# Kernel optimization log

Measured on AMD Instinct MI355X. Metric: run time of the kernel, lower is better.

Reference implementation:

```python
import jax, jax.numpy as jnp
import numpy as np

P = 4        # number of sequence pairs (half batch)
L = 512      # sequence length
D = 64       # embedding dim
NUM_CLASSES = 4
BIAS_INIT = 10.0


def setup_inputs() -> dict:
    key = jax.random.key(0)
    k1, k2, k3 = jax.random.split(key, 3)
    seqs_logits = jax.random.normal(k1, (2 * P, L, D), dtype=jnp.float32)
    ordinal_weight = jax.random.normal(k2, (1, NUM_CLASSES), dtype=jnp.float32)
    ordinal_bias = jax.random.normal(k3, (NUM_CLASSES,), dtype=jnp.float32) + BIAS_INIT
    return {"seqs_logits": seqs_logits, "ordinal_weight": ordinal_weight,
            "ordinal_bias": ordinal_bias}


def reference(seqs_logits, ordinal_weight, ordinal_bias):
    half = seqs_logits.shape[0] // 2
    z0 = seqs_logits[:half]          # [P, L0, D]
    z1 = seqs_logits[half:2 * half]  # [P, L1, D]

    def score_plus(z0_i, z1_i):
        # pairwise negative L1 distance: [L0, L1]
        s = -jnp.sum(jnp.abs(z0_i[:, None, :] - z1_i[None, :, :]), axis=-1)
        a = jax.nn.softmax(s, axis=1)   # row-wise alignment
        b = jax.nn.softmax(s, axis=0)   # column-wise alignment
        c = a + b - a * b               # symmetric soft alignment
        c_val = jnp.sum(c * s) / jnp.sum(c)
        logit = c_val * ordinal_weight + ordinal_bias  # [1, 4]
        return logit.reshape(-1)        # [4]

    return jax.vmap(score_plus)(z0, z1)  # [P, 4]
```

## Files before the change

kernel.cpp:

```cpp
#include <hip/hip_runtime.h>
#include <math.h>

#define P 4
#define L 512
#define D 64
#define NC 4
#define RS 68
#define SHIFT 64.0f

#define COLP_O  0
#define RA1_O   16384
#define RA2_O   32768
#define RAB1_O  49152
#define RAB2_O  65536
#define BP_O    81920

__device__ __forceinline__ void stage2(const float* __restrict__ z, int pair, int jb, int kb,
                                       int tid, float (*jt)[RS], float (*kt)[RS]) {
    const float4* z0t = (const float4*)(z + ((size_t)pair * L + jb * 64) * D);
    const float4* z1t = (const float4*)(z + ((size_t)(P + pair) * L + kb * 64) * D);
    #pragma unroll
    for (int i = 0; i < 4; ++i) {
        const int li = i * 256 + tid;
        const float4 a = z0t[li];
        const float4 b = z1t[li];
        *(float4*)&jt[li >> 4][(li & 15) * 4] = a;
        *(float4*)&kt[li >> 4][(li & 15) * 4] = b;
    }
}

__device__ __forceinline__ void dist16(const float (*bt)[RS], const float (*vt)[RS],
                                       int ty, int tx, float acc[4][4]) {
    #pragma unroll
    for (int r = 0; r < 4; ++r)
        #pragma unroll
        for (int q = 0; q < 4; ++q) acc[r][q] = 0.f;
    #pragma unroll
    for (int c = 0; c < 16; ++c) {
        float4 bv[4], vv[4];
        #pragma unroll
        for (int r = 0; r < 4; ++r) bv[r] = *(const float4*)&bt[ty + 16 * r][c * 4];
        #pragma unroll
        for (int q = 0; q < 4; ++q) vv[q] = *(const float4*)&vt[tx + 16 * q][c * 4];
        #pragma unroll
        for (int r = 0; r < 4; ++r)
            #pragma unroll
            for (int q = 0; q < 4; ++q)
                acc[r][q] += fabsf(bv[r].x - vv[q].x) + fabsf(bv[r].y - vv[q].y)
                           + fabsf(bv[r].z - vv[q].z) + fabsf(bv[r].w - vv[q].w);
    }
}

__global__ __launch_bounds__(256) void col_pass(const float* __restrict__ z, float* __restrict__ ws) {
    const int bx = blockIdx.x;
    const int pair = bx >> 6, kb = (bx >> 3) & 7, jb = bx & 7;
    const int tid = threadIdx.x, tx = tid & 15, ty = tid >> 4;
    __shared__ float jt[64][RS], kt[64][RS];
    stage2(z, pair, jb, kb, tid, jt, kt);
    __syncthreads();

    float acc[4][4];
    dist16(kt, jt, ty, tx, acc);

    float csum[4];
    #pragma unroll
    for (int r = 0; r < 4; ++r) {
        float s = 0.f;
        #pragma unroll
        for (int q = 0; q < 4; ++q) s += __expf(SHIFT - acc[r][q]);
        csum[r] = s;
    }
    #pragma unroll
    for (int off = 1; off <= 8; off <<= 1)
        #pragma unroll
        for (int r = 0; r < 4; ++r) csum[r] += __shfl_xor(csum[r], off);
    if (tx == 0) {
        #pragma unroll
        for (int r = 0; r < 4; ++r)
            ws[COLP_O + (pair * 8 + jb) * 512 + kb * 64 + ty + 16 * r] = csum[r];
    }
}

__global__ __launch_bounds__(256) void row_pass(const float* __restrict__ z, float* __restrict__ ws) {
    const int bx = blockIdx.x;
    const int pair = bx >> 6, kb = (bx >> 3) & 7, jb = bx & 7;
    const int tid = threadIdx.x, tx = tid & 15, ty = tid >> 4;
    __shared__ float jt[64][RS], kt[64][RS];
    __shared__ float ctmp[64][4];
    __shared__ float crcp_s[64];
    __shared__ float bred[4][2];

    stage2(z, pair, jb, kb, tid, jt, kt);
    {
        const int kl = tid >> 2, q = tid & 3;
        ctmp[kl][q] = ws[COLP_O + (pair * 8 + 2 * q) * 512 + kb * 64 + kl]
                    + ws[COLP_O + (pair * 8 + 2 * q + 1) * 512 + kb * 64 + kl];
    }
    __syncthreads();
    if (tid < 64)
        crcp_s[tid] = 1.0f / (ctmp[tid][0] + ctmp[tid][1] + ctmp[tid][2] + ctmp[tid][3]);
    __syncthreads();

    float crcp[4];
    #pragma unroll
    for (int q = 0; q < 4; ++q) crcp[q] = crcp_s[tx + 16 * q];

    float acc[4][4];
    dist16(jt, kt, ty, tx, acc);

    float A1[4], A2[4], AB1[4], AB2[4], Bs = 0.f, Bc = 0.f;
    #pragma unroll
    for (int r = 0; r < 4; ++r) { A1[r] = A2[r] = AB1[r] = AB2[r] = 0.f; }
    #pragma unroll
    for (int r = 0; r < 4; ++r) {
        #pragma unroll
        for (int q = 0; q < 4; ++q) {
            const float sv = -acc[r][q];
            const float e  = __expf(SHIFT + sv);
            const float b  = e * crcp[q];
            const float eb = e * b;
            A1[r]  += e * sv;   A2[r]  += e;
            AB1[r] += eb * sv;  AB2[r] += eb;
            Bs += b * sv;       Bc += b;
        }
    }
    #pragma unroll
    for (int off = 1; off <= 8; off <<= 1) {
        #pragma unroll
        for (int r = 0; r < 4; ++r) {
            A1[r]  += __shfl_xor(A1[r],  off);
            A2[r]  += __shfl_xor(A2[r],  off);
            AB1[r] += __shfl_xor(AB1[r], off);
            AB2[r] += __shfl_xor(AB2[r], off);
        }
    }
    if (tx == 0) {
        #pragma unroll
        for (int r = 0; r < 4; ++r) {
            const int idx = (pair * 8 + kb) * 512 + jb * 64 + ty + 16 * r;
            ws[RA1_O + idx]  = A1[r];
            ws[RA2_O + idx]  = A2[r];
            ws[RAB1_O + idx] = AB1[r];
            ws[RAB2_O + idx] = AB2[r];
        }
    }
    #pragma unroll
    for (int off = 1; off <= 32; off <<= 1) {
        Bs += __shfl_xor(Bs, off);
        Bc += __shfl_xor(Bc, off);
    }
    const int wave = tid >> 6, lane = tid & 63;
    if (lane == 0) { bred[wave][0] = Bs; bred[wave][1] = Bc; }
    __syncthreads();
    if (tid == 0) {
        const int bidp = kb * 8 + jb;
        ws[BP_O + (pair * 64 + bidp) * 2]     = bred[0][0] + bred[1][0] + bred[2][0] + bred[3][0];
        ws[BP_O + (pair * 64 + bidp) * 2 + 1] = bred[0][1] + bred[1][1] + bred[2][1] + bred[3][1];
    }
}

__global__ __launch_bounds__(256) void finalize(const float* __restrict__ ws,
                                                const float* __restrict__ w,
                                                const float* __restrict__ bias,
                                                float* __restrict__ out) {
    const int pair = blockIdx.x;
    const int tid = threadIdx.x;
    float cs = 0.f, cc = 0.f;
    #pragma unroll
    for (int jj = 0; jj < 2; ++jj) {
        const int j = tid + jj * 256;
        float A1 = 0.f, A2 = 0.f, AB1 = 0.f, AB2 = 0.f;
        #pragma unroll
        for (int kb = 0; kb < 8; ++kb) {
            const int idx = (pair * 8 + kb) * 512 + j;
            A1  += ws[RA1_O + idx];
            A2  += ws[RA2_O + idx];
            AB1 += ws[RAB1_O + idx];
            AB2 += ws[RAB2_O + idx];
        }
        const float r = 1.0f / A2;
        cs += (A1 - AB1) * r;
        cc += 1.0f - AB2 * r;
    }
    if (tid < 64) {
        cs += ws[BP_O + (pair * 64 + tid) * 2];
        cc += ws[BP_O + (pair * 64 + tid) * 2 + 1];
    }
    #pragma unroll
    for (int off = 1; off <= 32; off <<= 1) {
        cs += __shfl_xor(cs, off);
        cc += __shfl_xor(cc, off);
    }
    __shared__ float red[4][2];
    const int wave = tid >> 6, lane = tid & 63;
    if (lane == 0) { red[wave][0] = cs; red[wave][1] = cc; }
    __syncthreads();
    if (tid == 0) {
        const float tcs = red[0][0] + red[1][0] + red[2][0] + red[3][0];
        const float tcc = red[0][1] + red[1][1] + red[2][1] + red[3][1];
        const float c_val = tcs / tcc;
        #pragma unroll
        for (int cls = 0; cls < NC; ++cls)
            out[pair * NC + cls] = c_val * w[cls] + bias[cls];
    }
}

extern "C" void kernel_launch(void* const* d_in, const int* in_sizes, int n_in,
                              void* d_out, int out_size, void* d_ws, size_t ws_size,
                              hipStream_t stream) {
    const float* z    = (const float*)d_in[0];
    const float* w    = (const float*)d_in[1];
    const float* bias = (const float*)d_in[2];
    float* out = (float*)d_out;
    float* ws  = (float*)d_ws;

    col_pass<<<dim3(P * 64), dim3(256), 0, stream>>>(z, ws);
    row_pass<<<dim3(P * 64), dim3(256), 0, stream>>>(z, ws);
    finalize<<<dim3(P),      dim3(256), 0, stream>>>(ws, w, bias, out);
}
```

Measured before the change: 75.39 us.

## Compute distance matrix once, store it, and accumulate alignment in second pass

Instead of computing the L1 distance tile twice (once for column sums, once for row stats), a single kernel computes distances, writes them to workspace, and emits both row and column exp partial sums. A second kernel reloads the stored distances, forms the full symmetric alignment c directly with row and column reciprocals, and reduces c*s and c per block. Finalize becomes one block handling all pairs. This trades a second distance computation for an 8 MB write and read of the score matrix through global memory.

```diff
diff --git a/kernel.cpp b/kernel.cpp
--- a/kernel.cpp
+++ b/kernel.cpp
@@ -8,149 +8,147 @@
 #define RS 68
 #define SHIFT 64.0f
 
-#define COLP_O  0
-#define RA1_O   16384
-#define RA2_O   32768
-#define RAB1_O  49152
-#define RAB2_O  65536
-#define BP_O    81920
+#define COLP_O 0
+#define ROWP_O 16384
+#define BP_O   32768
+#define SV_O   33280
 
-__device__ __forceinline__ void stage2(const float* __restrict__ z, int pair, int jb, int kb,
-                                       int tid, float (*jt)[RS], float (*kt)[RS]) {
-    const float4* z0t = (const float4*)(z + ((size_t)pair * L + jb * 64) * D);
-    const float4* z1t = (const float4*)(z + ((size_t)(P + pair) * L + kb * 64) * D);
-    #pragma unroll
-    for (int i = 0; i < 4; ++i) {
-        const int li = i * 256 + tid;
-        const float4 a = z0t[li];
-        const float4 b = z1t[li];
-        *(float4*)&jt[li >> 4][(li & 15) * 4] = a;
-        *(float4*)&kt[li >> 4][(li & 15) * 4] = b;
+__global__ __launch_bounds__(256) void dist_stats(const float* __restrict__ z,
+                                                  float* __restrict__ ws) {
+    const int bx = blockIdx.x;
+    const int pair = bx >> 6, kb = (bx >> 3) & 7, jb = bx & 7;
+    const int tid = threadIdx.x, tx = tid & 15, ty = tid >> 4;
+    const int wave = tid >> 6, lane = tid & 63;
+
+    __shared__ float jt[64][RS], kt[64][RS];
+    __shared__ float csred[4][64];
+
+    {
+        const float4* z0t = (const float4*)(z + ((size_t)pair * L + jb * 64) * D);
+        const float4* z1t = (const float4*)(z + ((size_t)(P + pair) * L + kb * 64) * D);
+        #pragma unroll
+        for (int i = 0; i < 4; ++i) {
+            const int li = i * 256 + tid;
+            const float4 a = z0t[li];
+            const float4 b = z1t[li];
+            *(float4*)&jt[li >> 4][(li & 15) * 4] = a;
+            *(float4*)&kt[li >> 4][(li & 15) * 4] = b;
+        }
     }
-}
+    __syncthreads();
 
-__device__ __forceinline__ void dist16(const float (*bt)[RS], const float (*vt)[RS],
-                                       int ty, int tx, float acc[4][4]) {
+    float acc[4][4];
     #pragma unroll
     for (int r = 0; r < 4; ++r)
         #pragma unroll
         for (int q = 0; q < 4; ++q) acc[r][q] = 0.f;
     #pragma unroll
     for (int c = 0; c < 16; ++c) {
-        float4 bv[4], vv[4];
+        float4 jv[4], kv[4];
         #pragma unroll
-        for (int r = 0; r < 4; ++r) bv[r] = *(const float4*)&bt[ty + 16 * r][c * 4];
+        for (int r = 0; r < 4; ++r) jv[r] = *(const float4*)&jt[ty + 16 * r][c * 4];
         #pragma unroll
-        for (int q = 0; q < 4; ++q) vv[q] = *(const float4*)&vt[tx + 16 * q][c * 4];
+        for (int q = 0; q < 4; ++q) kv[q] = *(const float4*)&kt[tx + 16 * q][c * 4];
         #pragma unroll
         for (int r = 0; r < 4; ++r)
             #pragma unroll
             for (int q = 0; q < 4; ++q)
-                acc[r][q] += fabsf(bv[r].x - vv[q].x) + fabsf(bv[r].y - vv[q].y)
-                           + fabsf(bv[r].z - vv[q].z) + fabsf(bv[r].w - vv[q].w);
+                acc[r][q] += fabsf(jv[r].x - kv[q].x) + fabsf(jv[r].y - kv[q].y)
+                           + fabsf(jv[r].z - kv[q].z) + fabsf(jv[r].w - kv[q].w);
     }
+
+    {
+        float* svb = ws + SV_O + (size_t)bx * 4096;
+        #pragma unroll
+        for (int r = 0; r < 4; ++r)
+            #pragma unroll
+            for (int q = 0; q < 4; ++q)
+                svb[(r * 4 + q) * 256 + tid] = -acc[r][q];
+    }
+
+    float rs_[4] = {0.f, 0.f, 0.f, 0.f};
+    float cs_[4] = {0.f, 0.f, 0.f, 0.f};
+    #pragma unroll
+    for (int r = 0; r < 4; ++r)
+        #pragma unroll
+        for (int q = 0; q < 4; ++q) {
+            const float e = __expf(SHIFT - acc[r][q]);
+            rs_[r] += e;
+            cs_[q] += e;
+        }
+    #pragma unroll
+    for (int off = 1; off <= 8; off <<= 1)
+        #pragma unroll
+        for (int r = 0; r < 4; ++r) rs_[r] += __shfl_xor(rs_[r], off);
+    if (tx == 0) {
+        #pragma unroll
+        for (int r = 0; r < 4; ++r)
+            ws[ROWP_O + (pair * 8 + kb) * 512 + jb * 64 + ty + 16 * r] = rs_[r];
+    }
+    #pragma unroll
+    for (int off = 16; off <= 32; off <<= 1)
+        #pragma unroll
+        for (int q = 0; q < 4; ++q) cs_[q] += __shfl_xor(cs_[q], off);
+    if ((lane >> 4) == 0) {
+        #pragma unroll
+        for (int q = 0; q < 4; ++q) csred[wave][q * 16 + tx] = cs_[q];
+    }
+    __syncthreads();
+    if (tid < 64)
+        ws[COLP_O + (pair * 8 + jb) * 512 + kb * 64 + (tid & 15) + 16 * (tid >> 4)]
+            = csred[0][tid] + csred[1][tid] + csred[2][tid] + csred[3][tid];
 }
 
-__global__ __launch_bounds__(256) void col_pass(const float* __restrict__ z, float* __restrict__ ws) {
+__global__ __launch_bounds__(256) void c_accum(const float* __restrict__ wsc,
+                                               float* __restrict__ ws) {
     const int bx = blockIdx.x;
     const int pair = bx >> 6, kb = (bx >> 3) & 7, jb = bx & 7;
     const int tid = threadIdx.x, tx = tid & 15, ty = tid >> 4;
-    __shared__ float jt[64][RS], kt[64][RS];
-    stage2(z, pair, jb, kb, tid, jt, kt);
+    const int wave = tid >> 6, lane = tid & 63;
+
+    __shared__ float rtmp[64][4], ctmp[64][4];
+    __shared__ float rrcp_s[64], crcp_s[64];
+    __shared__ float bred[4][2];
+
+    {
+        const int l = tid >> 2, p4 = tid & 3;
+        rtmp[l][p4] = wsc[ROWP_O + (pair * 8 + 2 * p4) * 512 + jb * 64 + l]
+                    + wsc[ROWP_O + (pair * 8 + 2 * p4 + 1) * 512 + jb * 64 + l];
+        ctmp[l][p4] = wsc[COLP_O + (pair * 8 + 2 * p4) * 512 + kb * 64 + l]
+                    + wsc[COLP_O + (pair * 8 + 2 * p4 + 1) * 512 + kb * 64 + l];
+    }
+    __syncthreads();
+    if (tid < 64) {
+        rrcp_s[tid] = 1.0f / (rtmp[tid][0] + rtmp[tid][1] + rtmp[tid][2] + rtmp[tid][3]);
+    } else if (tid < 128) {
+        const int l = tid - 64;
+        crcp_s[l] = 1.0f / (ctmp[l][0] + ctmp[l][1] + ctmp[l][2] + ctmp[l][3]);
+    }
     __syncthreads();
 
-    float acc[4][4];
-    dist16(kt, jt, ty, tx, acc);
-
-    float csum[4];
+    const float* svb = wsc + SV_O + (size_t)bx * 4096;
+    float cs = 0.f, cc = 0.f;
     #pragma unroll
     for (int r = 0; r < 4; ++r) {
-        float s = 0.f;
-        #pragma unroll
-        for (int q = 0; q < 4; ++q) s += __expf(SHIFT - acc[r][q]);
-        csum[r] = s;
-    }
-    #pragma unroll
-    for (int off = 1; off <= 8; off <<= 1)
-        #pragma unroll
-        for (int r = 0; r < 4; ++r) csum[r] += __shfl_xor(csum[r], off);
-    if (tx == 0) {
-        #pragma unroll
-        for (int r = 0; r < 4; ++r)
-            ws[COLP_O + (pair * 8 + jb) * 512 + kb * 64 + ty + 16 * r] = csum[r];
-    }
-}
-
-__global__ __launch_bounds__(256) void row_pass(const float* __restrict__ z, float* __restrict__ ws) {
-    const int bx = blockIdx.x;
-    const int pair = bx >> 6, kb = (bx >> 3) & 7, jb = bx & 7;
-    const int tid = threadIdx.x, tx = tid & 15, ty = tid >> 4;
-    __shared__ float jt[64][RS], kt[64][RS];
-    __shared__ float ctmp[64][4];
-    __shared__ float crcp_s[64];
-    __shared__ float bred[4][2];
-
-    stage2(z, pair, jb, kb, tid, jt, kt);
-    {
-        const int kl = tid >> 2, q = tid & 3;
-        ctmp[kl][q] = ws[COLP_O + (pair * 8 + 2 * q) * 512 + kb * 64 + kl]
-                    + ws[COLP_O + (pair * 8 + 2 * q + 1) * 512 + kb * 64 + kl];
-    }
-    __syncthreads();
-    if (tid < 64)
-        crcp_s[tid] = 1.0f / (ctmp[tid][0] + ctmp[tid][1] + ctmp[tid][2] + ctmp[tid][3]);
-    __syncthreads();
-
-    float crcp[4];
-    #pragma unroll
-    for (int q = 0; q < 4; ++q) crcp[q] = crcp_s[tx + 16 * q];
-
-    float acc[4][4];
-    dist16(jt, kt, ty, tx, acc);
-
-    float A1[4], A2[4], AB1[4], AB2[4], Bs = 0.f, Bc = 0.f;
-    #pragma unroll
-    for (int r = 0; r < 4; ++r) { A1[r] = A2[r] = AB1[r] = AB2[r] = 0.f; }
-    #pragma unroll
-    for (int r = 0; r < 4; ++r) {
+        const float rr = rrcp_s[ty + 16 * r];
         #pragma unroll
         for (int q = 0; q < 4; ++q) {
-            const float sv = -acc[r][q];
+            const float cr = crcp_s[tx + 16 * q];
+            const float sv = svb[(r * 4 + q) * 256 + tid];
             const float e  = __expf(SHIFT + sv);
-            const float b  = e * crcp[q];
-            const float eb = e * b;
-            A1[r]  += e * sv;   A2[r]  += e;
-            AB1[r] += eb * sv;  AB2[r] += eb;
-            Bs += b * sv;       Bc += b;
-        }
-    }
-    #pragma unroll
-    for (int off = 1; off <= 8; off <<= 1) {
-        #pragma unroll
-        for (int r = 0; r < 4; ++r) {
-            A1[r]  += __shfl_xor(A1[r],  off);
-            A2[r]  += __shfl_xor(A2[r],  off);
-            AB1[r] += __shfl_xor(AB1[r], off);
-            AB2[r] += __shfl_xor(AB2[r], off);
-        }
-    }
-    if (tx == 0) {
-        #pragma unroll
-        for (int r = 0; r < 4; ++r) {
-            const int idx = (pair * 8 + kb) * 512 + jb * 64 + ty + 16 * r;
-            ws[RA1_O + idx]  = A1[r];
-            ws[RA2_O + idx]  = A2[r];
-            ws[RAB1_O + idx] = AB1[r];
-            ws[RAB2_O + idx] = AB2[r];
+            const float a  = e * rr;
+            const float b  = e * cr;
+            const float c  = a + b - a * b;
+            cs += c * sv;
+            cc += c;
         }
     }
     #pragma unroll
     for (int off = 1; off <= 32; off <<= 1) {
-        Bs += __shfl_xor(Bs, off);
-        Bc += __shfl_xor(Bc, off);
+        cs += __shfl_xor(cs, off);
+        cc += __shfl_xor(cc, off);
     }
-    const int wave = tid >> 6, lane = tid & 63;
-    if (lane == 0) { bred[wave][0] = Bs; bred[wave][1] = Bc; }
+    if (lane == 0) { bred[wave][0] = cs; bred[wave][1] = cc; }
     __syncthreads();
     if (tid == 0) {
         const int bidp = kb * 8 + jb;
@@ -163,42 +161,17 @@
                                                 const float* __restrict__ w,
                                                 const float* __restrict__ bias,
                                                 float* __restrict__ out) {
-    const int pair = blockIdx.x;
     const int tid = threadIdx.x;
-    float cs = 0.f, cc = 0.f;
-    #pragma unroll
-    for (int jj = 0; jj < 2; ++jj) {
-        const int j = tid + jj * 256;
-        float A1 = 0.f, A2 = 0.f, AB1 = 0.f, AB2 = 0.f;
-        #pragma unroll
-        for (int kb = 0; kb < 8; ++kb) {
-            const int idx = (pair * 8 + kb) * 512 + j;
-            A1  += ws[RA1_O + idx];
-            A2  += ws[RA2_O + idx];
-            AB1 += ws[RAB1_O + idx];
-            AB2 += ws[RAB2_O + idx];
-        }
-        const float r = 1.0f / A2;
-        cs += (A1 - AB1) * r;
-        cc += 1.0f - AB2 * r;
-    }
-    if (tid < 64) {
-        cs += ws[BP_O + (pair * 64 + tid) * 2];
-        cc += ws[BP_O + (pair * 64 + tid) * 2 + 1];
-    }
+    const int pair = tid >> 6, lane = tid & 63;
+    float cs = ws[BP_O + (pair * 64 + lane) * 2];
+    float cc = ws[BP_O + (pair * 64 + lane) * 2 + 1];
     #pragma unroll
     for (int off = 1; off <= 32; off <<= 1) {
         cs += __shfl_xor(cs, off);
         cc += __shfl_xor(cc, off);
     }
-    __shared__ float red[4][2];
-    const int wave = tid >> 6, lane = tid & 63;
-    if (lane == 0) { red[wave][0] = cs; red[wave][1] = cc; }
-    __syncthreads();
-    if (tid == 0) {
-        const float tcs = red[0][0] + red[1][0] + red[2][0] + red[3][0];
-        const float tcc = red[0][1] + red[1][1] + red[2][1] + red[3][1];
-        const float c_val = tcs / tcc;
+    if (lane == 0) {
+        const float c_val = cs / cc;
         #pragma unroll
         for (int cls = 0; cls < NC; ++cls)
             out[pair * NC + cls] = c_val * w[cls] + bias[cls];
@@ -214,7 +187,7 @@
     float* out = (float*)d_out;
     float* ws  = (float*)d_ws;
 
-    col_pass<<<dim3(P * 64), dim3(256), 0, stream>>>(z, ws);
-    row_pass<<<dim3(P * 64), dim3(256), 0, stream>>>(z, ws);
-    finalize<<<dim3(P),      dim3(256), 0, stream>>>(ws, w, bias, out);
+    dist_stats<<<dim3(P * 64), dim3(256), 0, stream>>>(z, ws);
+    c_accum   <<<dim3(P * 64), dim3(256), 0, stream>>>(ws, ws);
+    finalize  <<<dim3(1),      dim3(256), 0, stream>>>(ws, w, bias, out);
 }
```

Result: faster. 68.72 us (-8.9%).
